# Kernel tuning notes

Hardware: AMD Instinct MI355X
Metric: run time of the kernel (lower is better)

The kernel has to match this reference:

```python
import jax, jax.numpy as jnp
import numpy as np

B, C, H, W_IMG, P, D = 64, 3, 224, 224, 16, 768
N_PATCH = (H // P) * (W_IMG // P)  # 196
SEQ = N_PATCH + 1                  # 197


def setup_inputs() -> dict:
    key = jax.random.key(0)
    k1, k2, k3, k4, k5 = jax.random.split(key, 5)
    in_feat = P * P * C  # 768
    return {
        "x": jax.random.normal(k1, (B, C, H, W_IMG), dtype=jnp.float32),
        "W": jax.random.normal(k2, (in_feat, D), dtype=jnp.float32) * (1.0 / np.sqrt(in_feat)),
        "b": jax.random.normal(k3, (D,), dtype=jnp.float32) * 0.02,
        "pos_table": jax.random.normal(k4, (SEQ, D), dtype=jnp.float32) * 0.02,
        "class_token": jax.random.normal(k5, (1, 1, D), dtype=jnp.float32),
    }


def _patchify(x):
    # Matches torch loop: patch (i,j) is x[:, :, i*P:(i+1)*P, j*P:(j+1)*P].reshape(B, C*P*P)
    # i.e. features ordered channel-major then row then col within patch.
    b = x.shape[0]
    hp, wp = H // P, W_IMG // P
    x = x.reshape(b, C, hp, P, wp, P)              # (B,C,hp,P,wp,P)
    x = x.transpose(0, 2, 4, 1, 3, 5)              # (B,hp,wp,C,P,P)
    return x.reshape(b, hp * wp, C * P * P)        # (B,N,C*P*P)


def reference(x, W, b, pos_table, class_token):
    patches = _patchify(x)                          # (B, N, C*P*P)
    tokens = jnp.einsum("bnf,fd->bnd", patches, W) + b  # (B, N, D)
    cls = jnp.broadcast_to(class_token, (x.shape[0], 1, D))
    seq = jnp.concatenate([cls, tokens], axis=1)    # (B, SEQ, D)
    # positions = arange(SEQ) broadcast over batch -> embedding lookup
    return seq + pos_table[None, :, :]              # dropout is identity in eval
```

## Files before the change

### kernel.cpp

```cpp
#include <hip/hip_runtime.h>
#include <hip/hip_bf16.h>

namespace {

constexpr int Bsz = 64, Cch = 3, Himg = 224, Wimg = 224, Ppat = 16;
constexpr int Dm = 768, NPW = 14, NPATCH = 196, SEQn = 197;
constexpr int Mtot = Bsz * NPATCH;
constexpr int Ktot = 768, Ntot = 768;
constexpr int BM = 64, BN = 128, BK = 64;
constexpr int MT = Mtot / BM;
constexpr int NT = Ntot / BN;
constexpr int KT = Ktot / BK;
constexpr int NBLK = MT * NT;
constexpr int TA = BM * BK;
constexpr int TB = BN * BK;
constexpr size_t AP_ELEMS = (size_t)MT * KT * TA;
constexpr size_t WT_ELEMS = (size_t)NT * KT * TB;
constexpr size_t WS_NEED = (AP_ELEMS + WT_ELEMS) * 2;
constexpr int PATCH_BLK = MT * KT;
constexpr int WPREP_BLK = (Ktot / 8) * Ntot / 256;
constexpr int CLS_BLK = Bsz * Dm / 256;

typedef __attribute__((ext_vector_type(8))) short bf16x8;
typedef __attribute__((ext_vector_type(4))) float f32x4;

__device__ inline unsigned short f2bf(float f) {
  __bf16 h = (__bf16)f;
  union { __bf16 h; unsigned short u; } c;
  c.h = h;
  return c.u;
}

union Pack8 { unsigned short s[8]; uint4 v; };

__global__ void prep_kernel(const float* __restrict__ x, const float* __restrict__ W,
                            const float* __restrict__ pos, const float* __restrict__ cls,
                            unsigned short* __restrict__ Ap, unsigned short* __restrict__ Wt,
                            float* __restrict__ out, int nPatchBlk) {
  const int bid = blockIdx.x;
  const int t = threadIdx.x;
  if (bid < nPatchBlk) {
    int mt = bid / KT, kt = bid - mt * KT;
    int r = t >> 2, ks = t & 3;
    int m = mt * BM + r;
    int b = m / NPATCH;
    int pidx = m - b * NPATCH;
    int ph = pidx / NPW, pw = pidx - ph * NPW;
    int kg = kt * BK + ks * 16;
    int c = kg >> 8, pi = (kg >> 4) & 15;
    const float* src = x + ((size_t)(b * Cch + c) * Himg + ph * Ppat + pi) * Wimg
                       + pw * Ppat;
    float4 v0 = *reinterpret_cast<const float4*>(src + 0);
    float4 v1 = *reinterpret_cast<const float4*>(src + 4);
    float4 v2 = *reinterpret_cast<const float4*>(src + 8);
    float4 v3 = *reinterpret_cast<const float4*>(src + 12);
    Pack8 p0, p1;
    p0.s[0] = f2bf(v0.x); p0.s[1] = f2bf(v0.y); p0.s[2] = f2bf(v0.z); p0.s[3] = f2bf(v0.w);
    p0.s[4] = f2bf(v1.x); p0.s[5] = f2bf(v1.y); p0.s[6] = f2bf(v1.z); p0.s[7] = f2bf(v1.w);
    p1.s[0] = f2bf(v2.x); p1.s[1] = f2bf(v2.y); p1.s[2] = f2bf(v2.z); p1.s[3] = f2bf(v2.w);
    p1.s[4] = f2bf(v3.x); p1.s[5] = f2bf(v3.y); p1.s[6] = f2bf(v3.z); p1.s[7] = f2bf(v3.w);
    unsigned short* dst = Ap + (size_t)bid * TA;
    int g = r * BK + ks * 16;
    int sw = (r & 7) << 3;
    *reinterpret_cast<uint4*>(dst + (g ^ sw)) = p0.v;
    *reinterpret_cast<uint4*>(dst + ((g + 8) ^ sw)) = p1.v;
  } else if (bid < nPatchBlk + WPREP_BLK) {
    int cid = (bid - nPatchBlk) * 256 + t;
    int kc = cid / Ntot;
    int n = cid - kc * Ntot;
    int nb = n >> 7;
    int np = n & 127;
    int kt = kc >> 3;
    int k8 = (kc & 7) * 8;
    Pack8 p;
#pragma unroll
    for (int j = 0; j < 8; ++j) p.s[j] = f2bf(W[(size_t)(kc * 8 + j) * Ntot + n]);
    int sidx = (np * BK + k8) ^ ((np & 7) << 3);
    *reinterpret_cast<uint4*>(Wt + (size_t)(nb * KT + kt) * TB + sidx) = p.v;
  } else {
    int i = (bid - nPatchBlk - WPREP_BLK) * 256 + t;
    int b = i / Dm;
    int d = i - b * Dm;
    out[(size_t)b * (SEQn * Dm) + d] = cls[d] + pos[d];
  }
}

__global__ __launch_bounds__(256, 6)
void gemm_kernel(const unsigned short* __restrict__ Ap, const unsigned short* __restrict__ Wt,
                 const float* __restrict__ bias, const float* __restrict__ pos,
                 float* __restrict__ out) {
  __shared__ unsigned short A[TA];
  __shared__ unsigned short B[TB];

  const int orig = blockIdx.x;
  const int wg = (orig & 7) * (NBLK / 8) + (orig >> 3);
  const int bm = wg / NT;
  const int bn = wg - bm * NT;

  const int t = threadIdx.x;
  const int lane = t & 63;
  const int wid = t >> 6;
  const int wr = wid >> 1, wc = wid & 1;
  const int fr = lane & 15, fq = lane >> 4;

  const unsigned short* aSrc = Ap + (size_t)(bm * KT) * TA + t * 8;
  const unsigned short* bSrc = Wt + (size_t)(bn * KT) * TB + t * 8;

  auto STAGE = [&](int kt) {
#pragma unroll
    for (int i = 0; i < 2; ++i)
      __builtin_amdgcn_global_load_lds(
          (const __attribute__((address_space(1))) unsigned int*)(aSrc + kt * TA + i * 2048),
          (__attribute__((address_space(3))) unsigned int*)(&A[t * 8 + i * 2048]),
          16, 0, 0);
#pragma unroll
    for (int i = 0; i < 4; ++i)
      __builtin_amdgcn_global_load_lds(
          (const __attribute__((address_space(1))) unsigned int*)(bSrc + kt * TB + i * 2048),
          (__attribute__((address_space(3))) unsigned int*)(&B[t * 8 + i * 2048]),
          16, 0, 0);
  };

  f32x4 acc[2][4];
#pragma unroll
  for (int mi = 0; mi < 2; ++mi)
#pragma unroll
    for (int ni = 0; ni < 4; ++ni) acc[mi][ni] = {0.f, 0.f, 0.f, 0.f};

  for (int kt = 0; kt < KT; ++kt) {
    STAGE(kt);
    __syncthreads();
#pragma unroll
    for (int ks = 0; ks < 2; ++ks) {
      bf16x8 af[2], bfr[4];
#pragma unroll
      for (int mi = 0; mi < 2; ++mi) {
        int row = wr * 32 + mi * 16 + fr;
        int idx = (row * BK + ks * 32 + fq * 8) ^ ((row & 7) << 3);
        af[mi] = *reinterpret_cast<const bf16x8*>(&A[idx]);
      }
#pragma unroll
      for (int ni = 0; ni < 4; ++ni) {
        int n = wc * 64 + ni * 16 + fr;
        int idx = (n * BK + ks * 32 + fq * 8) ^ ((n & 7) << 3);
        bfr[ni] = *reinterpret_cast<const bf16x8*>(&B[idx]);
      }
#pragma unroll
      for (int mi = 0; mi < 2; ++mi)
#pragma unroll
        for (int ni = 0; ni < 4; ++ni)
          acc[mi][ni] = __builtin_amdgcn_mfma_f32_16x16x32_bf16(
              af[mi], bfr[ni], acc[mi][ni], 0, 0, 0);
    }
    if (kt + 1 < KT) __syncthreads();
  }

  const int n0 = bn * BN + wc * 64;
  float bv[4];
#pragma unroll
  for (int ni = 0; ni < 4; ++ni) bv[ni] = bias[n0 + ni * 16 + fr];
#pragma unroll
  for (int mi = 0; mi < 2; ++mi) {
#pragma unroll
    for (int j = 0; j < 4; ++j) {
      int m = bm * BM + wr * 32 + mi * 16 + fq * 4 + j;
      int b = m / NPATCH;
      int s = m - b * NPATCH + 1;
      float* orow = out + ((size_t)b * SEQn + s) * Dm + n0;
      const float* prow = pos + (size_t)s * Dm + n0;
#pragma unroll
      for (int ni = 0; ni < 4; ++ni) {
        int d = ni * 16 + fr;
        orow[d] = acc[mi][ni][j] + bv[ni] + prow[d];
      }
    }
  }
}

__global__ __launch_bounds__(512, 6)
void gemm_fb(const float* __restrict__ x, const unsigned short* __restrict__ Wt,
             const float* __restrict__ bias, const float* __restrict__ pos,
             float* __restrict__ out) {
  __shared__ unsigned short As[2][TA];
  __shared__ unsigned short Bs[2][TB];

  const int orig = blockIdx.x;
  const int wg = (orig & 7) * (NBLK / 8) + (orig >> 3);
  const int bm = wg / NT;
  const int bn = wg - bm * NT;

  const int t = threadIdx.x;
  const int lane = t & 63;
  const int wid = t >> 6;
  const int wr = wid >> 2, wc = wid & 3;
  const int fr = lane & 15, fq = lane >> 4;

  const int c4 = t & 15;
  const int r0 = t >> 4;
  int a_base[2];
#pragma unroll
  for (int i = 0; i < 2; ++i) {
    int m = bm * BM + r0 + 32 * i;
    int b = m / NPATCH;
    int pidx = m - b * NPATCH;
    int ph = pidx / NPW;
    int pw = pidx - ph * NPW;
    a_base[i] = ((b * Cch) * Himg + ph * Ppat) * Wimg + pw * Ppat;
  }
  const unsigned short* wt_base = Wt + (size_t)bn * (KT * TB);

  float4 av[2];
  auto LOADA = [&](int kt) {
    int kg = kt * BK + c4 * 4;
    int c = kg >> 8, pi = (kg >> 4) & 15, pj = kg & 15;
    int off = (c * Himg + pi) * Wimg + pj;
#pragma unroll
    for (int i = 0; i < 2; ++i)
      av[i] = *reinterpret_cast<const float4*>(x + a_base[i] + off);
  };
  auto WRITEA = [&](int buf) {
#pragma unroll
    for (int i = 0; i < 2; ++i) {
      int row = r0 + 32 * i;
      int idx = (row * BK + c4 * 4) ^ ((row & 7) << 3);
      ushort4 pk = make_ushort4(f2bf(av[i].x), f2bf(av[i].y), f2bf(av[i].z), f2bf(av[i].w));
      *reinterpret_cast<ushort4*>(&As[buf][idx]) = pk;
    }
  };
  auto STAGEB = [&](int buf, int kt) {
    const unsigned short* src = wt_base + kt * TB + t * 8;
#pragma unroll
    for (int i = 0; i < 2; ++i) {
      __builtin_amdgcn_global_load_lds(
          (const __attribute__((address_space(1))) unsigned int*)(src + i * 4096),
          (__attribute__((address_space(3))) unsigned int*)(&Bs[buf][t * 8 + i * 4096]),
          16, 0, 0);
    }
  };

  f32x4 acc[2][2];
#pragma unroll
  for (int mi = 0; mi < 2; ++mi)
#pragma unroll
    for (int ni = 0; ni < 2; ++ni) acc[mi][ni] = {0.f, 0.f, 0.f, 0.f};

  LOADA(0);
  STAGEB(0, 0);
  WRITEA(0);
  __syncthreads();

  for (int kt = 0; kt < KT; ++kt) {
    const int cur = kt & 1, nxt = cur ^ 1;
    if (kt + 1 < KT) {
      LOADA(kt + 1);
      STAGEB(nxt, kt + 1);
    }
#pragma unroll
    for (int ks = 0; ks < 2; ++ks) {
      bf16x8 af[2], bfr[2];
#pragma unroll
      for (int mi = 0; mi < 2; ++mi) {
        int row = wr * 32 + mi * 16 + fr;
        int idx = (row * BK + ks * 32 + fq * 8) ^ ((row & 7) << 3);
        af[mi] = *reinterpret_cast<const bf16x8*>(&As[cur][idx]);
      }
#pragma unroll
      for (int ni = 0; ni < 2; ++ni) {
        int n = wc * 32 + ni * 16 + fr;
        int idx = (n * BK + ks * 32 + fq * 8) ^ ((n & 7) << 3);
        bfr[ni] = *reinterpret_cast<const bf16x8*>(&Bs[cur][idx]);
      }
#pragma unroll
      for (int mi = 0; mi < 2; ++mi)
#pragma unroll
        for (int ni = 0; ni < 2; ++ni)
          acc[mi][ni] = __builtin_amdgcn_mfma_f32_16x16x32_bf16(
              af[mi], bfr[ni], acc[mi][ni], 0, 0, 0);
    }
    if (kt + 1 < KT) WRITEA(nxt);
    __syncthreads();
  }

  const int n0 = bn * BN + wc * 32;
  float bv[2];
#pragma unroll
  for (int ni = 0; ni < 2; ++ni) bv[ni] = bias[n0 + ni * 16 + fr];
#pragma unroll
  for (int mi = 0; mi < 2; ++mi) {
#pragma unroll
    for (int j = 0; j < 4; ++j) {
      int m = bm * BM + wr * 32 + mi * 16 + fq * 4 + j;
      int b = m / NPATCH;
      int s = m - b * NPATCH + 1;
      float* orow = out + ((size_t)b * SEQn + s) * Dm + n0;
      const float* prow = pos + (size_t)s * Dm + n0;
#pragma unroll
      for (int ni = 0; ni < 2; ++ni) {
        int d = ni * 16 + fr;
        orow[d] = acc[mi][ni][j] + bv[ni] + prow[d];
      }
    }
  }
}

}

extern "C" void kernel_launch(void* const* d_in, const int* in_sizes, int n_in,
                              void* d_out, int out_size, void* d_ws, size_t ws_size,
                              hipStream_t stream) {
  const float* x = (const float*)d_in[0];
  const float* W = (const float*)d_in[1];
  const float* bias = (const float*)d_in[2];
  const float* pos = (const float*)d_in[3];
  const float* cls = (const float*)d_in[4];
  float* out = (float*)d_out;

  const bool pure = ws_size >= WS_NEED;
  unsigned short* Ap = (unsigned short*)d_ws;
  unsigned short* Wt = pure ? Ap + AP_ELEMS : Ap;
  const int nPatchBlk = pure ? PATCH_BLK : 0;

  prep_kernel<<<nPatchBlk + WPREP_BLK + CLS_BLK, 256, 0, stream>>>(
      x, W, pos, cls, Ap, Wt, out, nPatchBlk);
  if (pure)
    gemm_kernel<<<NBLK, 256, 0, stream>>>(Ap, Wt, bias, pos, out);
  else
    gemm_fb<<<NBLK, 512, 0, stream>>>(x, Wt, bias, pos, out);
}
```

Before: 40.18 us.

## Load W fragments directly from global into registers, bypassing LDS for B

The weight tile is no longer staged through shared memory. The prep kernel now stores W in a plain per-k-slab layout with no swizzle, and each wave reads its bf16x8 MFMA B fragments straight from global memory into registers. The A tile load is software-prefetched one step ahead, issued after the closing barrier. This cuts LDS traffic and space for B, but each wave now pays global/L2 latency on its B loads, which are duplicated across waves sharing a column, and it uses more registers. The fallback kernel is reshaped to 256 threads to match.

```diff
diff --git a/kernel.cpp b/kernel.cpp
--- a/kernel.cpp
+++ b/kernel.cpp
@@ -13,9 +13,9 @@
 constexpr int KT = Ktot / BK;
 constexpr int NBLK = MT * NT;
 constexpr int TA = BM * BK;
-constexpr int TB = BN * BK;
+constexpr int KSLAB = Ntot * BK;
 constexpr size_t AP_ELEMS = (size_t)MT * KT * TA;
-constexpr size_t WT_ELEMS = (size_t)NT * KT * TB;
+constexpr size_t WT_ELEMS = (size_t)KT * KSLAB;
 constexpr size_t WS_NEED = (AP_ELEMS + WT_ELEMS) * 2;
 constexpr int PATCH_BLK = MT * KT;
 constexpr int WPREP_BLK = (Ktot / 8) * Ntot / 256;
@@ -68,15 +68,12 @@
     int cid = (bid - nPatchBlk) * 256 + t;
     int kc = cid / Ntot;
     int n = cid - kc * Ntot;
-    int nb = n >> 7;
-    int np = n & 127;
     int kt = kc >> 3;
-    int k8 = (kc & 7) * 8;
+    int kk = kc & 7;
     Pack8 p;
 #pragma unroll
     for (int j = 0; j < 8; ++j) p.s[j] = f2bf(W[(size_t)(kc * 8 + j) * Ntot + n]);
-    int sidx = (np * BK + k8) ^ ((np & 7) << 3);
-    *reinterpret_cast<uint4*>(Wt + (size_t)(nb * KT + kt) * TB + sidx) = p.v;
+    *reinterpret_cast<uint4*>(Wt + (size_t)kt * KSLAB + (size_t)n * BK + kk * 8) = p.v;
   } else {
     int i = (bid - nPatchBlk - WPREP_BLK) * 256 + t;
     int b = i / Dm;
@@ -85,12 +82,11 @@
   }
 }
 
-__global__ __launch_bounds__(256, 6)
+__global__ __launch_bounds__(256, 5)
 void gemm_kernel(const unsigned short* __restrict__ Ap, const unsigned short* __restrict__ Wt,
                  const float* __restrict__ bias, const float* __restrict__ pos,
                  float* __restrict__ out) {
   __shared__ unsigned short A[TA];
-  __shared__ unsigned short B[TB];
 
   const int orig = blockIdx.x;
   const int wg = (orig & 7) * (NBLK / 8) + (orig >> 3);
@@ -104,21 +100,15 @@
   const int fr = lane & 15, fq = lane >> 4;
 
   const unsigned short* aSrc = Ap + (size_t)(bm * KT) * TA + t * 8;
-  const unsigned short* bSrc = Wt + (size_t)(bn * KT) * TB + t * 8;
-
-  auto STAGE = [&](int kt) {
+  const unsigned short* bBase = Wt + (size_t)(bn * BN + wc * 64 + fr) * BK + fq * 8;
+
+  auto STAGE_A = [&](int kt) {
 #pragma unroll
     for (int i = 0; i < 2; ++i)
       __builtin_amdgcn_global_load_lds(
           (const __attribute__((address_space(1))) unsigned int*)(aSrc + kt * TA + i * 2048),
           (__attribute__((address_space(3))) unsigned int*)(&A[t * 8 + i * 2048]),
           16, 0, 0);
-#pragma unroll
-    for (int i = 0; i < 4; ++i)
-      __builtin_amdgcn_global_load_lds(
-          (const __attribute__((address_space(1))) unsigned int*)(bSrc + kt * TB + i * 2048),
-          (__attribute__((address_space(3))) unsigned int*)(&B[t * 8 + i * 2048]),
-          16, 0, 0);
   };
 
   f32x4 acc[2][4];
@@ -127,12 +117,20 @@
 #pragma unroll
     for (int ni = 0; ni < 4; ++ni) acc[mi][ni] = {0.f, 0.f, 0.f, 0.f};
 
+  STAGE_A(0);
+#pragma unroll
   for (int kt = 0; kt < KT; ++kt) {
-    STAGE(kt);
+    const unsigned short* bP = bBase + (size_t)kt * KSLAB;
+    bf16x8 breg[2][4];
+#pragma unroll
+    for (int ks = 0; ks < 2; ++ks)
+#pragma unroll
+      for (int ni = 0; ni < 4; ++ni)
+        breg[ks][ni] = *reinterpret_cast<const bf16x8*>(bP + ni * 16 * BK + ks * 32);
     __syncthreads();
 #pragma unroll
     for (int ks = 0; ks < 2; ++ks) {
-      bf16x8 af[2], bfr[4];
+      bf16x8 af[2];
 #pragma unroll
       for (int mi = 0; mi < 2; ++mi) {
         int row = wr * 32 + mi * 16 + fr;
@@ -140,19 +138,16 @@
         af[mi] = *reinterpret_cast<const bf16x8*>(&A[idx]);
       }
 #pragma unroll
-      for (int ni = 0; ni < 4; ++ni) {
-        int n = wc * 64 + ni * 16 + fr;
-        int idx = (n * BK + ks * 32 + fq * 8) ^ ((n & 7) << 3);
-        bfr[ni] = *reinterpret_cast<const bf16x8*>(&B[idx]);
-      }
-#pragma unroll
       for (int mi = 0; mi < 2; ++mi)
 #pragma unroll
         for (int ni = 0; ni < 4; ++ni)
           acc[mi][ni] = __builtin_amdgcn_mfma_f32_16x16x32_bf16(
-              af[mi], bfr[ni], acc[mi][ni], 0, 0, 0);
-    }
-    if (kt + 1 < KT) __syncthreads();
+              af[mi], breg[ks][ni], acc[mi][ni], 0, 0, 0);
+    }
+    if (kt + 1 < KT) {
+      __syncthreads();
+      STAGE_A(kt + 1);
+    }
   }
 
   const int n0 = bn * BN + wc * 64;
@@ -177,12 +172,11 @@
   }
 }
 
-__global__ __launch_bounds__(512, 6)
+__global__ __launch_bounds__(256, 2)
 void gemm_fb(const float* __restrict__ x, const unsigned short* __restrict__ Wt,
              const float* __restrict__ bias, const float* __restrict__ pos,
              float* __restrict__ out) {
   __shared__ unsigned short As[2][TA];
-  __shared__ unsigned short Bs[2][TB];
 
   const int orig = blockIdx.x;
   const int wg = (orig & 7) * (NBLK / 8) + (orig >> 3);
@@ -192,72 +186,66 @@
   const int t = threadIdx.x;
   const int lane = t & 63;
   const int wid = t >> 6;
-  const int wr = wid >> 2, wc = wid & 3;
+  const int wr = wid >> 1, wc = wid & 1;
   const int fr = lane & 15, fq = lane >> 4;
 
   const int c4 = t & 15;
   const int r0 = t >> 4;
-  int a_base[2];
-#pragma unroll
-  for (int i = 0; i < 2; ++i) {
-    int m = bm * BM + r0 + 32 * i;
+  int a_base[4];
+#pragma unroll
+  for (int i = 0; i < 4; ++i) {
+    int m = bm * BM + r0 + 16 * i;
     int b = m / NPATCH;
     int pidx = m - b * NPATCH;
     int ph = pidx / NPW;
     int pw = pidx - ph * NPW;
     a_base[i] = ((b * Cch) * Himg + ph * Ppat) * Wimg + pw * Ppat;
   }
-  const unsigned short* wt_base = Wt + (size_t)bn * (KT * TB);
-
-  float4 av[2];
+
+  float4 av[4];
   auto LOADA = [&](int kt) {
     int kg = kt * BK + c4 * 4;
     int c = kg >> 8, pi = (kg >> 4) & 15, pj = kg & 15;
     int off = (c * Himg + pi) * Wimg + pj;
 #pragma unroll
-    for (int i = 0; i < 2; ++i)
+    for (int i = 0; i < 4; ++i)
       av[i] = *reinterpret_cast<const float4*>(x + a_base[i] + off);
   };
   auto WRITEA = [&](int buf) {
 #pragma unroll
-    for (int i = 0; i < 2; ++i) {
-      int row = r0 + 32 * i;
+    for (int i = 0; i < 4; ++i) {
+      int row = r0 + 16 * i;
       int idx = (row * BK + c4 * 4) ^ ((row & 7) << 3);
       ushort4 pk = make_ushort4(f2bf(av[i].x), f2bf(av[i].y), f2bf(av[i].z), f2bf(av[i].w));
       *reinterpret_cast<ushort4*>(&As[buf][idx]) = pk;
     }
   };
-  auto STAGEB = [&](int buf, int kt) {
-    const unsigned short* src = wt_base + kt * TB + t * 8;
-#pragma unroll
-    for (int i = 0; i < 2; ++i) {
-      __builtin_amdgcn_global_load_lds(
-          (const __attribute__((address_space(1))) unsigned int*)(src + i * 4096),
-          (__attribute__((address_space(3))) unsigned int*)(&Bs[buf][t * 8 + i * 4096]),
-          16, 0, 0);
-    }
-  };
-
-  f32x4 acc[2][2];
+
+  const unsigned short* bBase = Wt + (size_t)(bn * BN + wc * 64 + fr) * BK + fq * 8;
+
+  f32x4 acc[2][4];
 #pragma unroll
   for (int mi = 0; mi < 2; ++mi)
 #pragma unroll
-    for (int ni = 0; ni < 2; ++ni) acc[mi][ni] = {0.f, 0.f, 0.f, 0.f};
+    for (int ni = 0; ni < 4; ++ni) acc[mi][ni] = {0.f, 0.f, 0.f, 0.f};
 
   LOADA(0);
-  STAGEB(0, 0);
   WRITEA(0);
   __syncthreads();
 
   for (int kt = 0; kt < KT; ++kt) {
     const int cur = kt & 1, nxt = cur ^ 1;
-    if (kt + 1 < KT) {
-      LOADA(kt + 1);
-      STAGEB(nxt, kt + 1);
-    }
+    if (kt + 1 < KT) LOADA(kt + 1);
+    const unsigned short* bP = bBase + (size_t)kt * KSLAB;
+    bf16x8 breg[2][4];
+#pragma unroll
+    for (int ks = 0; ks < 2; ++ks)
+#pragma unroll
+      for (int ni = 0; ni < 4; ++ni)
+        breg[ks][ni] = *reinterpret_cast<const bf16x8*>(bP + ni * 16 * BK + ks * 32);
 #pragma unroll
     for (int ks = 0; ks < 2; ++ks) {
-      bf16x8 af[2], bfr[2];
+      bf16x8 af[2];
 #pragma unroll
       for (int mi = 0; mi < 2; ++mi) {
         int row = wr * 32 + mi * 16 + fr;
@@ -265,26 +253,20 @@
         af[mi] = *reinterpret_cast<const bf16x8*>(&As[cur][idx]);
       }
 #pragma unroll
-      for (int ni = 0; ni < 2; ++ni) {
-        int n = wc * 32 + ni * 16 + fr;
-        int idx = (n * BK + ks * 32 + fq * 8) ^ ((n & 7) << 3);
-        bfr[ni] = *reinterpret_cast<const bf16x8*>(&Bs[cur][idx]);
-      }
-#pragma unroll
       for (int mi = 0; mi < 2; ++mi)
 #pragma unroll
-        for (int ni = 0; ni < 2; ++ni)
+        for (int ni = 0; ni < 4; ++ni)
           acc[mi][ni] = __builtin_amdgcn_mfma_f32_16x16x32_bf16(
-              af[mi], bfr[ni], acc[mi][ni], 0, 0, 0);
+              af[mi], breg[ks][ni], acc[mi][ni], 0, 0, 0);
     }
     if (kt + 1 < KT) WRITEA(nxt);
     __syncthreads();
   }
 
-  const int n0 = bn * BN + wc * 32;
-  float bv[2];
-#pragma unroll
-  for (int ni = 0; ni < 2; ++ni) bv[ni] = bias[n0 + ni * 16 + fr];
+  const int n0 = bn * BN + wc * 64;
+  float bv[4];
+#pragma unroll
+  for (int ni = 0; ni < 4; ++ni) bv[ni] = bias[n0 + ni * 16 + fr];
 #pragma unroll
   for (int mi = 0; mi < 2; ++mi) {
 #pragma unroll
@@ -295,7 +277,7 @@
       float* orow = out + ((size_t)b * SEQn + s) * Dm + n0;
       const float* prow = pos + (size_t)s * Dm + n0;
 #pragma unroll
-      for (int ni = 0; ni < 2; ++ni) {
+      for (int ni = 0; ni < 4; ++ni) {
         int d = ni * 16 + fr;
         orow[d] = acc[mi][ni][j] + bv[ni] + prow[d];
       }
@@ -325,5 +307,5 @@
   if (pure)
     gemm_kernel<<<NBLK, 256, 0, stream>>>(Ap, Wt, bias, pos, out);
   else
-    gemm_fb<<<NBLK, 512, 0, stream>>>(x, Wt, bias, pos, out);
-}
+    gemm_fb<<<NBLK, 256, 0, stream>>>(x, Wt, bias, pos, out);
+}
```

Measured after the change: 81.27 us. 2.02x slower.
